# Kernel tuning notes

Measured on AMD Instinct MI355X. Metric: run time of the kernel, lower is better.

Reference implementation:

```python
import jax, jax.numpy as jnp
import numpy as np

B, H, L, D = 2, 8, 512, 64
TEMP = 8.0  # sqrt(D)


def setup_inputs() -> dict:
    key = jax.random.key(0)
    ks = jax.random.split(key, 6)
    q = jax.random.normal(ks[0], (B, H, L, D), jnp.float32)
    k = jax.random.normal(ks[1], (B, H, L, D), jnp.float32)
    v = jax.random.normal(ks[2], (B, H, L, D), jnp.float32)
    adj_k = jax.random.normal(ks[3], (B, L, L, D), jnp.float32)
    adj_v = jax.random.normal(ks[4], (B, L, L, D), jnp.float32)
    mask = jax.random.randint(ks[5], (B, 1, 1, L), 0, 2, jnp.int32)
    return {"q": q, "k": k, "v": v, "adj_k": adj_k, "adj_v": adj_v, "mask": mask}


def reference(q, k, v, adj_k, adj_v, mask):
    qs = q / TEMP
    # standard QK^T term + relation term: score[b,h,i,j] += q[b,h,i]. adj_k[b,i,j]
    attn = jnp.einsum('bhid,bhjd->bhij', qs, k) + jnp.einsum('bhid,bijd->bhij', qs, adj_k)
    attn = jnp.where(mask == 0, jnp.float32(-10000.0), attn)
    attn = jax.nn.softmax(attn, axis=-1)  # dropout p=0 (eval / deterministic)
    # standard AV term + relation term: out[b,h,i] += sum_j attn[b,h,i,j]*adj_v[b,i,j]
    out = jnp.einsum('bhij,bhjd->bhid', attn, v) + jnp.einsum('bhij,bijd->bhid', attn, adj_v)
    return out, attn
```

## Files before the change

### kernel.cpp

```cpp
#include <hip/hip_runtime.h>

constexpr int B  = 2;
constexpr int NH = 8;
constexpr int L  = 512;
constexpr int D  = 64;
constexpr float INV_TEMP = 0.125f;

__global__ __launch_bounds__(256) void k1_qk(const float* __restrict__ q,
                                             const float* __restrict__ k,
                                             float* __restrict__ s1) {
  const int bh = blockIdx.x, it = blockIdx.y, jt = blockIdx.z;
  __shared__ float Qs[64][68];
  __shared__ float Ks[64][68];
  const int t = threadIdx.x;
  const float* qb = q + ((size_t)bh * L + it * 64) * D;
  const float* kb = k + ((size_t)bh * L + jt * 64) * D;
#pragma unroll
  for (int n0 = 0; n0 < 4; ++n0) {
    int n = t + (n0 << 8);
    int r = n >> 4, c = (n & 15) << 2;
    float4 a = *(const float4*)(qb + (size_t)r * D + c);
    a.x *= INV_TEMP; a.y *= INV_TEMP; a.z *= INV_TEMP; a.w *= INV_TEMP;
    *(float4*)&Qs[r][c] = a;
    *(float4*)&Ks[r][c] = *(const float4*)(kb + (size_t)r * D + c);
  }
  __syncthreads();
  const int i0 = t >> 4, j0 = t & 15;
  float acc[4][4] = {};
#pragma unroll 1
  for (int kc = 0; kc < 64; kc += 4) {
    float4 a[4], b[4];
#pragma unroll
    for (int m = 0; m < 4; ++m) a[m] = *(const float4*)&Qs[i0 + 16 * m][kc];
#pragma unroll
    for (int n = 0; n < 4; ++n) b[n] = *(const float4*)&Ks[j0 + 16 * n][kc];
#pragma unroll
    for (int m = 0; m < 4; ++m)
#pragma unroll
      for (int n = 0; n < 4; ++n)
        acc[m][n] = fmaf(a[m].x, b[n].x,
                    fmaf(a[m].y, b[n].y,
                    fmaf(a[m].z, b[n].z,
                    fmaf(a[m].w, b[n].w, acc[m][n]))));
  }
  float* sb = s1 + ((size_t)bh * L + it * 64) * L + jt * 64;
#pragma unroll
  for (int m = 0; m < 4; ++m) {
    float* srow = sb + (size_t)(i0 + 16 * m) * L;
#pragma unroll
    for (int n = 0; n < 4; ++n) srow[j0 + 16 * n] = acc[m][n];
  }
}

__global__ __launch_bounds__(512, 4) void k2_fused(
    const float* __restrict__ q, const float* __restrict__ adj_k,
    const float* __restrict__ adj_v, const int* __restrict__ mask,
    const float* __restrict__ s1, float* __restrict__ out,
    float* __restrict__ attn) {
  const int b = blockIdx.x >> 9, i = blockIdx.x & (L - 1);
  const int t = threadIdx.x;
  const int lane = t & 63;
  const int w = __builtin_amdgcn_readfirstlane(t >> 6);
  const int jb = w << 6;
  __shared__ float sc[NH][L];

  {
    const float* akr = adj_k + (((size_t)b * L + i) * L + jb + lane) * D;
    float4 row[16];
#pragma unroll
    for (int dc = 0; dc < 16; ++dc) row[dc] = *(const float4*)(akr + 4 * dc);
    const int mv = mask[b * L + jb + lane];
    float acc[NH];
#pragma unroll
    for (int h = 0; h < NH; ++h) {
      const float* qh = q + (((size_t)b * NH + h) * L + i) * D;
      float a0 = 0.f, a1 = 0.f;
#pragma unroll
      for (int dc = 0; dc < 16; dc += 2) {
        float4 q4 = *(const float4*)(qh + 4 * dc);
        float4 q5 = *(const float4*)(qh + 4 * dc + 4);
        a0 = fmaf(q4.x, row[dc].x, fmaf(q4.y, row[dc].y,
             fmaf(q4.z, row[dc].z, fmaf(q4.w, row[dc].w, a0))));
        a1 = fmaf(q5.x, row[dc + 1].x, fmaf(q5.y, row[dc + 1].y,
             fmaf(q5.z, row[dc + 1].z, fmaf(q5.w, row[dc + 1].w, a1))));
      }
      acc[h] = a0 + a1;
    }
#pragma unroll
    for (int h = 0; h < NH; ++h) {
      float s = s1[(((size_t)b * NH + h) * L + i) * L + jb + lane]
                + acc[h] * INV_TEMP;
      sc[h][jb + lane] = (mv == 0) ? -10000.0f : s;
    }
  }
  __syncthreads();

  {
    float* arow = attn + (((size_t)b * NH + w) * L + i) * L;
    float vals[8];
    float mx = -3.4e38f;
#pragma unroll
    for (int m = 0; m < 8; ++m) {
      float s = sc[w][lane + (m << 6)];
      vals[m] = s;
      mx = fmaxf(mx, s);
    }
#pragma unroll
    for (int off = 32; off > 0; off >>= 1) mx = fmaxf(mx, __shfl_xor(mx, off, 64));
    float sum = 0.f;
#pragma unroll
    for (int m = 0; m < 8; ++m) { vals[m] = __expf(vals[m] - mx); sum += vals[m]; }
#pragma unroll
    for (int off = 32; off > 0; off >>= 1) sum += __shfl_xor(sum, off, 64);
    const float inv = 1.0f / sum;
#pragma unroll
    for (int m = 0; m < 8; ++m) {
      int jj = lane + (m << 6);
      float p = vals[m] * inv;
      arow[jj] = p;
      sc[w][jj] = p;
    }
  }
  __syncthreads();

  {
    const int js = lane >> 4, dq = lane & 15;
    const float* avb = adj_v + ((size_t)b * L + i) * (size_t)(L * D)
                             + (size_t)jb * D + 4 * dq;
    float4 o[NH];
#pragma unroll
    for (int h = 0; h < NH; ++h) o[h] = make_float4(0.f, 0.f, 0.f, 0.f);
#pragma unroll 4
    for (int jj = 0; jj < 64; jj += 4) {
      const float4 av = *(const float4*)(avb + (size_t)(jj + js) * D);
      const int j = jb + jj + js;
#pragma unroll
      for (int h = 0; h < NH; ++h) {
        float p = sc[h][j];
        o[h].x = fmaf(p, av.x, o[h].x);
        o[h].y = fmaf(p, av.y, o[h].y);
        o[h].z = fmaf(p, av.z, o[h].z);
        o[h].w = fmaf(p, av.w, o[h].w);
      }
    }
#pragma unroll
    for (int h = 0; h < NH; ++h) {
      o[h].x += __shfl_xor(o[h].x, 16, 64); o[h].x += __shfl_xor(o[h].x, 32, 64);
      o[h].y += __shfl_xor(o[h].y, 16, 64); o[h].y += __shfl_xor(o[h].y, 32, 64);
      o[h].z += __shfl_xor(o[h].z, 16, 64); o[h].z += __shfl_xor(o[h].z, 32, 64);
      o[h].w += __shfl_xor(o[h].w, 16, 64); o[h].w += __shfl_xor(o[h].w, 32, 64);
    }
    __syncthreads();
    float* opart = &sc[0][0];
    if (js == 0) {
#pragma unroll
      for (int h = 0; h < NH; ++h)
        *(float4*)(opart + (((w << 3) + h) << 6) + 4 * dq) = o[h];
    }
    __syncthreads();
    float r = 0.f;
#pragma unroll
    for (int wv = 0; wv < 8; ++wv) r += opart[(((wv << 3) + w) << 6) + lane];
    out[(((size_t)b * NH + w) * L + i) * D + lane] = r;
  }
}

__global__ __launch_bounds__(256) void k3_av(const float* __restrict__ attn,
                                             const float* __restrict__ v,
                                             float* __restrict__ out) {
  const int bh = blockIdx.x, it = blockIdx.y;
  __shared__ float As[32][68];
  __shared__ float Vt[64][65];
  const int t = threadIdx.x;
  const float* ab = attn + ((size_t)bh * L + it * 32) * L;
  const float* vb = v + (size_t)bh * (size_t)(L * D);
  const int i0 = t >> 4, j0 = t & 15;
  float acc[2][4] = {};
#pragma unroll 1
  for (int jc = 0; jc < L; jc += 64) {
    __syncthreads();
#pragma unroll
    for (int n0 = 0; n0 < 2; ++n0) {
      int n = t + (n0 << 8);
      int r = n >> 4, c = (n & 15) << 2;
      *(float4*)&As[r][c] = *(const float4*)(ab + (size_t)r * L + jc + c);
    }
#pragma unroll
    for (int n0 = 0; n0 < 4; ++n0) {
      int n = t + (n0 << 8);
      int r = n >> 4, c = (n & 15) << 2;
      float4 a = *(const float4*)(vb + (size_t)(jc + r) * D + c);
      Vt[c][r] = a.x; Vt[c + 1][r] = a.y; Vt[c + 2][r] = a.z; Vt[c + 3][r] = a.w;
    }
    __syncthreads();
#pragma unroll 1
    for (int kc = 0; kc < 64; kc += 4) {
      float4 a[2];
#pragma unroll
      for (int m = 0; m < 2; ++m) a[m] = *(const float4*)&As[i0 + 16 * m][kc];
      float bb[4][4];
#pragma unroll
      for (int n = 0; n < 4; ++n) {
        const float* vr = &Vt[j0 + 16 * n][kc];
        bb[n][0] = vr[0]; bb[n][1] = vr[1]; bb[n][2] = vr[2]; bb[n][3] = vr[3];
      }
#pragma unroll
      for (int m = 0; m < 2; ++m)
#pragma unroll
        for (int n = 0; n < 4; ++n)
          acc[m][n] = fmaf(a[m].x, bb[n][0],
                      fmaf(a[m].y, bb[n][1],
                      fmaf(a[m].z, bb[n][2],
                      fmaf(a[m].w, bb[n][3], acc[m][n]))));
    }
  }
  float* ob = out + ((size_t)bh * L + it * 32) * D;
#pragma unroll
  for (int m = 0; m < 2; ++m)
#pragma unroll
    for (int n = 0; n < 4; ++n) {
      float* p = ob + (size_t)(i0 + 16 * m) * D + j0 + 16 * n;
      *p += acc[m][n];
    }
}

extern "C" void kernel_launch(void* const* d_in, const int* in_sizes, int n_in,
                              void* d_out, int out_size, void* d_ws, size_t ws_size,
                              hipStream_t stream) {
  const float* q     = (const float*)d_in[0];
  const float* k     = (const float*)d_in[1];
  const float* v     = (const float*)d_in[2];
  const float* adj_k = (const float*)d_in[3];
  const float* adj_v = (const float*)d_in[4];
  const int*   mask  = (const int*)d_in[5];
  float* out  = (float*)d_out;
  float* attn = out + (size_t)B * NH * L * D;
  float* s1   = (float*)d_ws;

  dim3 g1(B * NH, L / 64, L / 64);
  k1_qk<<<g1, 256, 0, stream>>>(q, k, s1);
  k2_fused<<<B * L, 512, 0, stream>>>(q, adj_k, adj_v, mask, s1, out, attn);
  dim3 g3(B * NH, L / 32);
  k3_av<<<g3, 256, 0, stream>>>(attn, v, out);
}
```

Measured before the change: 332.7 us.

## Stage adj_k tiles through LDS with register prefetch, one head per wave

The adj_k scoring phase changes from each wave loading its own 64 rows into registers and computing all 8 heads, to the whole block cooperatively staging 64-row adj_k tiles into shared memory. Each wave then computes its own head across all columns, and the next tile plus its s1 and mask values are prefetched in registers. The goal is coalesced adj_k reads, lower register pressure (a 64-float row array per thread is removed), and overlap of global loads with compute. In exchange it adds eight tile iterations with two block barriers each. The adj_v loop unroll is also raised from 4 to 8.

```diff
diff --git a/kernel.cpp b/kernel.cpp
--- a/kernel.cpp
+++ b/kernel.cpp
@@ -61,39 +61,52 @@
   const int t = threadIdx.x;
   const int lane = t & 63;
   const int w = __builtin_amdgcn_readfirstlane(t >> 6);
-  const int jb = w << 6;
   __shared__ float sc[NH][L];
+  __shared__ float ak[64][68];
 
   {
-    const float* akr = adj_k + (((size_t)b * L + i) * L + jb + lane) * D;
-    float4 row[16];
-#pragma unroll
-    for (int dc = 0; dc < 16; ++dc) row[dc] = *(const float4*)(akr + 4 * dc);
-    const int mv = mask[b * L + jb + lane];
-    float acc[NH];
-#pragma unroll
-    for (int h = 0; h < NH; ++h) {
-      const float* qh = q + (((size_t)b * NH + h) * L + i) * D;
-      float a0 = 0.f, a1 = 0.f;
-#pragma unroll
-      for (int dc = 0; dc < 16; dc += 2) {
-        float4 q4 = *(const float4*)(qh + 4 * dc);
-        float4 q5 = *(const float4*)(qh + 4 * dc + 4);
-        a0 = fmaf(q4.x, row[dc].x, fmaf(q4.y, row[dc].y,
-             fmaf(q4.z, row[dc].z, fmaf(q4.w, row[dc].w, a0))));
-        a1 = fmaf(q5.x, row[dc + 1].x, fmaf(q5.y, row[dc + 1].y,
-             fmaf(q5.z, row[dc + 1].z, fmaf(q5.w, row[dc + 1].w, a1))));
-      }
-      acc[h] = a0 + a1;
-    }
-#pragma unroll
-    for (int h = 0; h < NH; ++h) {
-      float s = s1[(((size_t)b * NH + h) * L + i) * L + jb + lane]
-                + acc[h] * INV_TEMP;
-      sc[h][jb + lane] = (mv == 0) ? -10000.0f : s;
-    }
-  }
-  __syncthreads();
+    const float* akb = adj_k + ((size_t)b * L + i) * (size_t)(L * D);
+    const float* qh  = q  + (((size_t)b * NH + w) * L + i) * D;
+    const float* s1r = s1 + (((size_t)b * NH + w) * L + i) * L;
+    const int*   mr  = mask + b * L;
+
+    const int sr0 = t >> 4, scol = (t & 15) << 2, sr1 = sr0 + 32;
+    float4 pf0 = *(const float4*)(akb + (size_t)sr0 * D + scol);
+    float4 pf1 = *(const float4*)(akb + (size_t)sr1 * D + scol);
+    float s1pf = s1r[lane];
+    int   mpf  = mr[lane];
+
+    for (int jc = 0; jc < L; jc += 64) {
+      *(float4*)&ak[sr0][scol] = pf0;
+      *(float4*)&ak[sr1][scol] = pf1;
+      __syncthreads();
+      float s1v = s1pf;
+      int   mv  = mpf;
+      if (jc + 64 < L) {
+        const float* nb = akb + (size_t)(jc + 64) * D;
+        pf0  = *(const float4*)(nb + (size_t)sr0 * D + scol);
+        pf1  = *(const float4*)(nb + (size_t)sr1 * D + scol);
+        s1pf = s1r[jc + 64 + lane];
+        mpf  = mr[jc + 64 + lane];
+      }
+      __builtin_amdgcn_sched_barrier(0);
+      float acc0 = 0.f, acc1 = 0.f;
+#pragma unroll
+      for (int dc = 0; dc < D; dc += 8) {
+        float4 a0 = *(const float4*)&ak[lane][dc];
+        float4 a1 = *(const float4*)&ak[lane][dc + 4];
+        float4 q0 = *(const float4*)(qh + dc);
+        float4 q1 = *(const float4*)(qh + dc + 4);
+        acc0 = fmaf(q0.x, a0.x, fmaf(q0.y, a0.y,
+               fmaf(q0.z, a0.z, fmaf(q0.w, a0.w, acc0))));
+        acc1 = fmaf(q1.x, a1.x, fmaf(q1.y, a1.y,
+               fmaf(q1.z, a1.z, fmaf(q1.w, a1.w, acc1))));
+      }
+      float s = s1v + (acc0 + acc1) * INV_TEMP;
+      sc[w][jc + lane] = (mv == 0) ? -10000.0f : s;
+      __syncthreads();
+    }
+  }
 
   {
     float* arow = attn + (((size_t)b * NH + w) * L + i) * L;
@@ -124,13 +137,14 @@
   __syncthreads();
 
   {
+    const int jb = w << 6;
     const int js = lane >> 4, dq = lane & 15;
     const float* avb = adj_v + ((size_t)b * L + i) * (size_t)(L * D)
                              + (size_t)jb * D + 4 * dq;
     float4 o[NH];
 #pragma unroll
     for (int h = 0; h < NH; ++h) o[h] = make_float4(0.f, 0.f, 0.f, 0.f);
-#pragma unroll 4
+#pragma unroll 8
     for (int jj = 0; jj < 64; jj += 4) {
       const float4 av = *(const float4*)(avb + (size_t)(jj + js) * D);
       const int j = jb + jj + js;
```

Result: faster. 326.1 us (-2.0%).

## Stage adj_k through LDS with double-buffered prefetch and batch adj_v loads

Applied to the files above, without the earlier changes.

The relation-score phase of the fused kernel is restructured. Each wave now owns one head and walks all 512 keys in 8 chunks of 64. The block cooperatively loads each 64x64 adj_k tile into shared memory with coalesced float4 loads, prefetching two chunks ahead in registers, instead of every lane streaming its own 256-byte row and looping over all heads. The adj_v phase issues all 16 float4 loads up front before the FMA loop to expose memory-level parallelism. This costs an extra ~17KB of LDS per block, 16 additional block barriers and higher register pressure, which may reduce occupancy.

```diff
diff --git a/kernel.cpp b/kernel.cpp
--- a/kernel.cpp
+++ b/kernel.cpp
@@ -52,6 +52,33 @@
   }
 }
 
+#define K2_CHUNK(CC, BUF0, BUF1)                                              \
+  {                                                                           \
+    *(float4*)&ak[sr0][scol] = BUF0;                                          \
+    *(float4*)&ak[sr1][scol] = BUF1;                                          \
+    __syncthreads();                                                          \
+    if ((CC) + 2 < 8) {                                                       \
+      BUF0 = *(const float4*)(p0 + (size_t)((CC) + 2) * (64 * D));            \
+      BUF1 = *(const float4*)(p1 + (size_t)((CC) + 2) * (64 * D));            \
+    }                                                                         \
+    __builtin_amdgcn_sched_barrier(0);                                        \
+    float acc0 = 0.f, acc1 = 0.f;                                             \
+    _Pragma("unroll")                                                         \
+    for (int dc = 0; dc < D; dc += 8) {                                       \
+      float4 x0 = *(const float4*)&ak[lane][dc];                              \
+      float4 x1 = *(const float4*)&ak[lane][dc + 4];                          \
+      float4 q0 = *(const float4*)(qh + dc);                                  \
+      float4 q1 = *(const float4*)(qh + dc + 4);                              \
+      acc0 = fmaf(q0.x, x0.x, fmaf(q0.y, x0.y,                                \
+             fmaf(q0.z, x0.z, fmaf(q0.w, x0.w, acc0))));                      \
+      acc1 = fmaf(q1.x, x1.x, fmaf(q1.y, x1.y,                                \
+             fmaf(q1.z, x1.z, fmaf(q1.w, x1.w, acc1))));                      \
+    }                                                                         \
+    float s = s1v[CC] + (acc0 + acc1) * INV_TEMP;                             \
+    sc[w][((CC) << 6) + lane] = (mv[CC] == 0) ? -10000.0f : s;                \
+    __syncthreads();                                                          \
+  }
+
 __global__ __launch_bounds__(512, 4) void k2_fused(
     const float* __restrict__ q, const float* __restrict__ adj_k,
     const float* __restrict__ adj_v, const int* __restrict__ mask,
@@ -61,39 +88,39 @@
   const int t = threadIdx.x;
   const int lane = t & 63;
   const int w = __builtin_amdgcn_readfirstlane(t >> 6);
-  const int jb = w << 6;
   __shared__ float sc[NH][L];
+  __shared__ float ak[64][68];
 
   {
-    const float* akr = adj_k + (((size_t)b * L + i) * L + jb + lane) * D;
-    float4 row[16];
-#pragma unroll
-    for (int dc = 0; dc < 16; ++dc) row[dc] = *(const float4*)(akr + 4 * dc);
-    const int mv = mask[b * L + jb + lane];
-    float acc[NH];
-#pragma unroll
-    for (int h = 0; h < NH; ++h) {
-      const float* qh = q + (((size_t)b * NH + h) * L + i) * D;
-      float a0 = 0.f, a1 = 0.f;
-#pragma unroll
-      for (int dc = 0; dc < 16; dc += 2) {
-        float4 q4 = *(const float4*)(qh + 4 * dc);
-        float4 q5 = *(const float4*)(qh + 4 * dc + 4);
-        a0 = fmaf(q4.x, row[dc].x, fmaf(q4.y, row[dc].y,
-             fmaf(q4.z, row[dc].z, fmaf(q4.w, row[dc].w, a0))));
-        a1 = fmaf(q5.x, row[dc + 1].x, fmaf(q5.y, row[dc + 1].y,
-             fmaf(q5.z, row[dc + 1].z, fmaf(q5.w, row[dc + 1].w, a1))));
-      }
-      acc[h] = a0 + a1;
-    }
-#pragma unroll
-    for (int h = 0; h < NH; ++h) {
-      float s = s1[(((size_t)b * NH + h) * L + i) * L + jb + lane]
-                + acc[h] * INV_TEMP;
-      sc[h][jb + lane] = (mv == 0) ? -10000.0f : s;
-    }
-  }
-  __syncthreads();
+    const float* akb = adj_k + ((size_t)b * L + i) * (size_t)(L * D);
+    const float* qh  = q  + (((size_t)b * NH + w) * L + i) * D;
+    const float* s1r = s1 + (((size_t)b * NH + w) * L + i) * L;
+    const int*   mr  = mask + b * L;
+    const int sr0 = t >> 4, scol = (t & 15) << 2, sr1 = sr0 + 32;
+
+    float s1v[8]; int mv[8];
+#pragma unroll
+    for (int m = 0; m < 8; ++m) {
+      s1v[m] = s1r[(m << 6) + lane];
+      mv[m]  = mr[(m << 6) + lane];
+    }
+
+    const float* p0 = akb + (size_t)sr0 * D + scol;
+    const float* p1 = akb + (size_t)sr1 * D + scol;
+    float4 bufA0 = *(const float4*)(p0);
+    float4 bufA1 = *(const float4*)(p1);
+    float4 bufB0 = *(const float4*)(p0 + 64 * D);
+    float4 bufB1 = *(const float4*)(p1 + 64 * D);
+
+    K2_CHUNK(0, bufA0, bufA1)
+    K2_CHUNK(1, bufB0, bufB1)
+    K2_CHUNK(2, bufA0, bufA1)
+    K2_CHUNK(3, bufB0, bufB1)
+    K2_CHUNK(4, bufA0, bufA1)
+    K2_CHUNK(5, bufB0, bufB1)
+    K2_CHUNK(6, bufA0, bufA1)
+    K2_CHUNK(7, bufB0, bufB1)
+  }
 
   {
     float* arow = attn + (((size_t)b * NH + w) * L + i) * L;
@@ -124,23 +151,28 @@
   __syncthreads();
 
   {
+    const int jb = w << 6;
     const int js = lane >> 4, dq = lane & 15;
     const float* avb = adj_v + ((size_t)b * L + i) * (size_t)(L * D)
-                             + (size_t)jb * D + 4 * dq;
+                             + (size_t)(jb + js) * D + 4 * dq;
+    float4 av[16];
+#pragma unroll
+    for (int u = 0; u < 16; ++u)
+      av[u] = *(const float4*)(avb + (size_t)(u << 2) * D);
+    __builtin_amdgcn_sched_barrier(0);
     float4 o[NH];
 #pragma unroll
     for (int h = 0; h < NH; ++h) o[h] = make_float4(0.f, 0.f, 0.f, 0.f);
-#pragma unroll 4
-    for (int jj = 0; jj < 64; jj += 4) {
-      const float4 av = *(const float4*)(avb + (size_t)(jj + js) * D);
-      const int j = jb + jj + js;
+#pragma unroll
+    for (int u = 0; u < 16; ++u) {
+      const int j = jb + (u << 2) + js;
 #pragma unroll
       for (int h = 0; h < NH; ++h) {
         float p = sc[h][j];
-        o[h].x = fmaf(p, av.x, o[h].x);
-        o[h].y = fmaf(p, av.y, o[h].y);
-        o[h].z = fmaf(p, av.z, o[h].z);
-        o[h].w = fmaf(p, av.w, o[h].w);
+        o[h].x = fmaf(p, av[u].x, o[h].x);
+        o[h].y = fmaf(p, av[u].y, o[h].y);
+        o[h].z = fmaf(p, av[u].z, o[h].z);
+        o[h].w = fmaf(p, av[u].w, o[h].w);
       }
     }
 #pragma unroll
```

Measured after the change: 332.6 us. About the same (-0.1%).

## Split adj_k score pass into separate wide-grid kernel before softmax/adj_v kernel

Applied to the files above, without the earlier changes.

The fused per-row kernel is split in two. The first kernel streams adj_k tiles through shared memory on a grid of 1024x8 blocks of 256 threads, and adds the relation scores plus the mask into s1 in place. The second kernel reads s1 back for the softmax and the adj_v accumulation, and its adj_v loop unroll rises from 4 to 8. The aim is more parallelism and lower register pressure for the bandwidth-bound adj_k stream, at the cost of an extra kernel launch and an extra global round trip of s1 (about 16 MB written and read again).

```diff
diff --git a/kernel.cpp b/kernel.cpp
--- a/kernel.cpp
+++ b/kernel.cpp
@@ -52,56 +52,62 @@
   }
 }
 
-__global__ __launch_bounds__(512, 4) void k2_fused(
+__global__ __launch_bounds__(256) void k2a_adjk(
     const float* __restrict__ q, const float* __restrict__ adj_k,
-    const float* __restrict__ adj_v, const int* __restrict__ mask,
-    const float* __restrict__ s1, float* __restrict__ out,
-    float* __restrict__ attn) {
+    const int* __restrict__ mask, float* __restrict__ s1) {
   const int b = blockIdx.x >> 9, i = blockIdx.x & (L - 1);
-  const int t = threadIdx.x;
-  const int lane = t & 63;
+  const int jc = blockIdx.y << 6;
+  const int t = threadIdx.x, lane = t & 63;
   const int w = __builtin_amdgcn_readfirstlane(t >> 6);
-  const int jb = w << 6;
+  __shared__ float akt[64][68];
+
+  const float* akb = adj_k + ((size_t)b * L + i) * (size_t)(L * D)
+                           + (size_t)jc * D;
+#pragma unroll
+  for (int n0 = 0; n0 < 4; ++n0) {
+    int n = t + (n0 << 8);
+    int r = n >> 4, c = (n & 15) << 2;
+    *(float4*)&akt[r][c] = *(const float4*)(akb + (size_t)r * D + c);
+  }
+  __syncthreads();
+
+  const float* qh0 = q + (((size_t)b * NH + w    ) * L + i) * D;
+  const float* qh1 = q + (((size_t)b * NH + w + 4) * L + i) * D;
+  float a0 = 0.f, a1 = 0.f;
+#pragma unroll
+  for (int dc = 0; dc < D; dc += 4) {
+    float4 x  = *(const float4*)&akt[lane][dc];
+    float4 qa = *(const float4*)(qh0 + dc);
+    float4 qb = *(const float4*)(qh1 + dc);
+    a0 = fmaf(qa.x, x.x, fmaf(qa.y, x.y, fmaf(qa.z, x.z, fmaf(qa.w, x.w, a0))));
+    a1 = fmaf(qb.x, x.x, fmaf(qb.y, x.y, fmaf(qb.z, x.z, fmaf(qb.w, x.w, a1))));
+  }
+  const int jj = jc + lane;
+  const int mv = mask[b * L + jj];
+  float* p0 = s1 + (((size_t)b * NH + w    ) * L + i) * L + jj;
+  float* p1 = s1 + (((size_t)b * NH + w + 4) * L + i) * L + jj;
+  float v0 = *p0 + a0 * INV_TEMP;
+  float v1 = *p1 + a1 * INV_TEMP;
+  *p0 = (mv == 0) ? -10000.0f : v0;
+  *p1 = (mv == 0) ? -10000.0f : v1;
+}
+
+__global__ __launch_bounds__(512, 4) void k2b_sm_av(
+    const float* __restrict__ adj_v, const float* __restrict__ s1,
+    float* __restrict__ out, float* __restrict__ attn) {
+  const int b = blockIdx.x >> 9, i = blockIdx.x & (L - 1);
+  const int t = threadIdx.x, lane = t & 63;
+  const int w = __builtin_amdgcn_readfirstlane(t >> 6);
   __shared__ float sc[NH][L];
 
   {
-    const float* akr = adj_k + (((size_t)b * L + i) * L + jb + lane) * D;
-    float4 row[16];
-#pragma unroll
-    for (int dc = 0; dc < 16; ++dc) row[dc] = *(const float4*)(akr + 4 * dc);
-    const int mv = mask[b * L + jb + lane];
-    float acc[NH];
-#pragma unroll
-    for (int h = 0; h < NH; ++h) {
-      const float* qh = q + (((size_t)b * NH + h) * L + i) * D;
-      float a0 = 0.f, a1 = 0.f;
-#pragma unroll
-      for (int dc = 0; dc < 16; dc += 2) {
-        float4 q4 = *(const float4*)(qh + 4 * dc);
-        float4 q5 = *(const float4*)(qh + 4 * dc + 4);
-        a0 = fmaf(q4.x, row[dc].x, fmaf(q4.y, row[dc].y,
-             fmaf(q4.z, row[dc].z, fmaf(q4.w, row[dc].w, a0))));
-        a1 = fmaf(q5.x, row[dc + 1].x, fmaf(q5.y, row[dc + 1].y,
-             fmaf(q5.z, row[dc + 1].z, fmaf(q5.w, row[dc + 1].w, a1))));
-      }
-      acc[h] = a0 + a1;
-    }
-#pragma unroll
-    for (int h = 0; h < NH; ++h) {
-      float s = s1[(((size_t)b * NH + h) * L + i) * L + jb + lane]
-                + acc[h] * INV_TEMP;
-      sc[h][jb + lane] = (mv == 0) ? -10000.0f : s;
-    }
-  }
-  __syncthreads();
-
-  {
+    const float* s1r = s1 + (((size_t)b * NH + w) * L + i) * L;
     float* arow = attn + (((size_t)b * NH + w) * L + i) * L;
     float vals[8];
     float mx = -3.4e38f;
 #pragma unroll
     for (int m = 0; m < 8; ++m) {
-      float s = sc[w][lane + (m << 6)];
+      float s = s1r[lane + (m << 6)];
       vals[m] = s;
       mx = fmaxf(mx, s);
     }
@@ -124,13 +130,14 @@
   __syncthreads();
 
   {
+    const int jb = w << 6;
     const int js = lane >> 4, dq = lane & 15;
     const float* avb = adj_v + ((size_t)b * L + i) * (size_t)(L * D)
                              + (size_t)jb * D + 4 * dq;
     float4 o[NH];
 #pragma unroll
     for (int h = 0; h < NH; ++h) o[h] = make_float4(0.f, 0.f, 0.f, 0.f);
-#pragma unroll 4
+#pragma unroll 8
     for (int jj = 0; jj < 64; jj += 4) {
       const float4 av = *(const float4*)(avb + (size_t)(jj + js) * D);
       const int j = jb + jj + js;
@@ -239,7 +246,9 @@
 
   dim3 g1(B * NH, L / 64, L / 64);
   k1_qk<<<g1, 256, 0, stream>>>(q, k, s1);
-  k2_fused<<<B * L, 512, 0, stream>>>(q, adj_k, adj_v, mask, s1, out, attn);
+  dim3 g2a(B * L, L / 64);
+  k2a_adjk<<<g2a, 256, 0, stream>>>(q, adj_k, mask, s1);
+  k2b_sm_av<<<B * L, 512, 0, stream>>>(adj_v, s1, out, attn);
   dim3 g3(B * NH, L / 32);
   k3_av<<<g3, 256, 0, stream>>>(attn, v, out);
 }
```

New measurement: 333.6 us. Within noise of the previous version (+0.3%).
